# Optimization experiments

Hardware: AMD Instinct MI355X
Metric: run time of the kernel (lower is better)

## Reference

```python
import jax, jax.numpy as jnp
import numpy as np
from jax import lax

# Key identity used: modulating ALL weights of output channel o by s_o (with no bias
# inside the modulated conv, as in the source where F.conv2d(..., bias=None)) is
# mathematically identical to a plain conv followed by per-(batch, out_channel)
# scaling of the output. This collapses the per-sample Python loop into one conv.

def _upsample2x(x):
    # nearest-neighbor x2, matching F.interpolate(scale_factor=2) default mode
    return jnp.repeat(jnp.repeat(x, 2, axis=2), 2, axis=3)

def _conv(x, w):
    return lax.conv_general_dilated(
        x, w, window_strides=(1, 1), padding=[(1, 1), (1, 1)],
        dimension_numbers=("NCHW", "OIHW", "NCHW"))

def _modconv(x, style, w, fc_w, fc_b):
    # style_fc: [B, style_dim] -> [B, out_ch]
    s = style @ fc_w.T + fc_b          # [B, O]
    y = _conv(x, w)                    # [B, O, H, W]
    return y * s[:, :, None, None]


def setup_inputs() -> dict:
    key = jax.random.key(0)
    ks = jax.random.split(key, 16)
    B, SD = 8, 512
    chans = [(512, 256), (256, 128), (128, 64), (64, 64), (64, 64)]
    inp = {
        "x": jax.random.normal(ks[0], (B, 512, 8, 8), jnp.float32),
        "style": jax.random.normal(ks[1], (B, SD), jnp.float32),
    }
    for i, (ci, co) in enumerate(chans, start=1):
        inp[f"w{i}"] = jax.random.normal(ks[2 * i], (co, ci, 3, 3), jnp.float32) * (1.0 / np.sqrt(ci * 9))
        inp[f"fw{i}"] = jax.random.normal(ks[2 * i + 1], (co, SD), jnp.float32) * (1.0 / np.sqrt(SD))
        inp[f"fb{i}"] = jnp.ones((co,), jnp.float32)
    inp["wf"] = jax.random.normal(ks[12], (3, 64, 3, 3), jnp.float32) * (1.0 / np.sqrt(64 * 9))
    inp["bf"] = jnp.zeros((3,), jnp.float32)
    return inp


def reference(x, style, w1, fw1, fb1, w2, fw2, fb2, w3, fw3, fb3,
              w4, fw4, fb4, w5, fw5, fb5, wf, bf):
    x = _upsample2x(x)
    x = jax.nn.relu(_modconv(x, style, w1, fw1, fb1))
    x = _upsample2x(x)
    x = jax.nn.relu(_modconv(x, style, w2, fw2, fb2))
    x = _upsample2x(x)
    x = jax.nn.relu(_modconv(x, style, w3, fw3, fb3))
    x = _upsample2x(x)
    x = jax.nn.relu(_modconv(x, style, w4, fw4, fb4))
    x = _upsample2x(x)
    x = jax.nn.relu(_modconv(x, style, w5, fw5, fb5))
    x = _conv(x, wf) + bf[None, :, None, None]
    return x
```

## Files before the change

kernel.cpp:

```cpp
#include <hip/hip_runtime.h>
#include <hip/hip_bf16.h>
#include <cstddef>

typedef __bf16 bf16x8 __attribute__((ext_vector_type(8)));
typedef float f32x4 __attribute__((ext_vector_type(4)));

__global__ void prep_all_kernel(const float* __restrict__ x, __hip_bfloat16* __restrict__ act0,
                                const float* __restrict__ w1, __hip_bfloat16* __restrict__ o1,
                                const float* __restrict__ w2, __hip_bfloat16* __restrict__ o2,
                                const float* __restrict__ w3, __hip_bfloat16* __restrict__ o3,
                                const float* __restrict__ w4, __hip_bfloat16* __restrict__ o4,
                                const float* __restrict__ w5, __hip_bfloat16* __restrict__ o5,
                                const float* __restrict__ wf, __hip_bfloat16* __restrict__ of,
                                const float* __restrict__ style,
                                const float* __restrict__ fw1, const float* __restrict__ fb1,
                                const float* __restrict__ fw2, const float* __restrict__ fb2,
                                const float* __restrict__ fw3, const float* __restrict__ fb3,
                                const float* __restrict__ fw4, const float* __restrict__ fb4,
                                const float* __restrict__ fw5, const float* __restrict__ fb5,
                                float* __restrict__ S) {
    const int blk = blockIdx.x;
    if (blk < 1024) {
        int t = blk * 256 + threadIdx.x;
        int c = t & 511; int rest = t >> 9;
        int w = rest & 7; rest >>= 3; int h = rest & 7; int b = rest >> 3;
        act0[t] = __float2bfloat16(x[((b * 512 + c) * 8 + h) * 8 + w]);
    } else if (blk < 7620) {
        int t = (blk - 1024) * 256 + threadIdx.x;
        if (t >= 1688576) return;
        if (t < 1548288) {
            const float* w; __hip_bfloat16* o; int lgci, lgco;
            if      (t < 1179648) { w = w1; o = o1; lgci = 9; lgco = 8; }
            else if (t < 1474560) { t -= 1179648; w = w2; o = o2; lgci = 8; lgco = 7; }
            else                  { t -= 1474560; w = w3; o = o3; lgci = 7; lgco = 6; }
            int CI = 1 << lgci;
            int ci = t & (CI - 1);
            int co = (t >> lgci) & ((1 << lgco) - 1);
            int tap = t >> (lgci + lgco);
            o[t] = __float2bfloat16(w[((size_t)co * CI + ci) * 9 + tap]);
        } else if (t < 1679360) {
            int u = t - 1548288;
            const float* w; __hip_bfloat16* o;
            if (u < 65536) { w = w4; o = o4; }
            else           { u -= 65536; w = w5; o = o5; }
            int j   = u & 7;
            int ln  = (u >> 3) & 63;
            int ch  = (u >> 9) & 1;
            int nt  = (u >> 10) & 3;
            int tp  = (u >> 12) & 3;
            int cls = (u >> 14) & 3;
            int py = cls >> 1, px = cls & 1;
            int i = tp >> 1, jj = tp & 1;
            int co = nt * 16 + (ln & 15);
            int ci = ch * 32 + (ln >> 4) * 8 + j;
            int r0 = i * (1 + py), rc = py ? (2 - i) : (1 + i);
            int c0 = jj * (1 + px), cc = px ? (2 - jj) : (1 + jj);
            const float* wb = w + ((size_t)co * 64 + ci) * 9;
            float s = 0.f;
            for (int rr = 0; rr < rc; ++rr)
                for (int c2 = 0; c2 < cc; ++c2)
                    s += wb[(r0 + rr) * 3 + (c0 + c2)];
            o[u] = __float2bfloat16(s);
        } else {
            int u = t - 1679360;
            int j  = u & 7;
            int ln = (u >> 3) & 63;
            int ch = (u >> 9) & 1;
            int tap = u >> 10;
            int rr = ln & 15, qq = ln >> 4;
            int ci = ch * 32 + qq * 8 + j;
            float v = (rr < 3) ? wf[((size_t)rr * 64 + ci) * 9 + tap] : 0.f;
            of[u] = __float2bfloat16(v);
        }
    } else {
        int wvid = (blk - 7620) * 4 + (threadIdx.x >> 6);
        int lane = threadIdx.x & 63;
        const float* fw; const float* fb; int lg, sOff, local;
        if      (wvid < 2048) { fw = fw1; fb = fb1; lg = 8; sOff = 0;    local = wvid; }
        else if (wvid < 3072) { fw = fw2; fb = fb2; lg = 7; sOff = 2048; local = wvid - 2048; }
        else if (wvid < 3584) { fw = fw3; fb = fb3; lg = 6; sOff = 3072; local = wvid - 3072; }
        else if (wvid < 4096) { fw = fw4; fb = fb4; lg = 6; sOff = 3584; local = wvid - 3584; }
        else                  { fw = fw5; fb = fb5; lg = 6; sOff = 4096; local = wvid - 4096; }
        int b = local >> lg, o = local & ((1 << lg) - 1);
        const float* sb = style + b * 512;
        const float* fwo = fw + (size_t)o * 512;
        float p = 0.f;
        #pragma unroll
        for (int k = lane; k < 512; k += 64) p += sb[k] * fwo[k];
        #pragma unroll
        for (int off = 32; off > 0; off >>= 1) p += __shfl_down(p, off);
        if (lane == 0) S[sOff + local] = p + fb[o];
    }
}

template <int CI, int CO, int HS, int WS>
__launch_bounds__(512)
__global__ void conv_partial_kernel(const __hip_bfloat16* __restrict__ actIn,
                                    const __hip_bfloat16* __restrict__ wtr,
                                    float* __restrict__ Part) {
    constexpr int HO = HS * 2, WO = WS * 2;
    constexpr size_t sliceN = (size_t)8 * HO * WO * CO;
    const int tid = threadIdx.x;
    const int lane = tid & 63, wv = tid >> 6;
    const int r = lane & 15, q = lane >> 4;
    const int pw = WO / 16, ppb = (HO / 16) * pw;
    const int b = blockIdx.x / ppb;
    const int prest = blockIdx.x - b * ppb;
    const int ph = prest / pw, pwi = prest - ph * pw;
    const int oh0 = ph * 16, ow0 = pwi * 16;
    const int sh0 = oh0 >> 1, sw0 = ow0 >> 1;
    const int n0 = blockIdx.y * 64;
    const int ciOff = blockIdx.z * 64;

    __shared__ alignas(16) __hip_bfloat16 Tile[100 * 72];
    __shared__ alignas(16) __hip_bfloat16 Wlds[2][64 * 72];

    f32x4 acc[2][4];
    #pragma unroll
    for (int i = 0; i < 2; ++i)
        #pragma unroll
        for (int j = 0; j < 4; ++j) acc[i][j] = f32x4{0.f, 0.f, 0.f, 0.f};

    for (int i = tid; i < 800; i += 512) {
        int pix = i >> 3, koct = i & 7;
        int tr = pix / 10, tc2 = pix - tr * 10;
        int su = sh0 - 1 + tr, sv = sw0 - 1 + tc2;
        uint4 v = {0, 0, 0, 0};
        if (su >= 0 && su < HS && sv >= 0 && sv < WS)
            v = *(const uint4*)(actIn + ((size_t)((b * HS + su) * WS + sv) * CI + ciOff + koct * 8));
        *(uint4*)&Tile[pix * 72 + koct * 8] = v;
    }
    {
        int co = tid >> 3, koct = tid & 7;
        *(uint4*)&Wlds[0][co * 72 + koct * 8] =
            *(const uint4*)(wtr + ((size_t)(n0 + co)) * CI + ciOff + koct * 8);
    }
    __syncthreads();

    #pragma unroll 1
    for (int tap = 0; tap < 9; ++tap) {
        const bool pf = (tap < 8);
        uint4 wr0 = {0,0,0,0};
        if (pf) {
            int co0 = tid >> 3, k0 = tid & 7;
            wr0 = *(const uint4*)(wtr + ((size_t)(tap + 1) * CO + n0 + co0) * CI + ciOff + k0 * 8);
        }
        const int dyv = tap / 3;
        const int dxm1 = tap - dyv * 3 - 1;
        const int tc = ((r + dxm1) >> 1) + 1;
        int apix[2];
        #pragma unroll
        for (int mt = 0; mt < 2; ++mt)
            apix[mt] = ((((wv * 2 + mt) + dyv - 1) >> 1) + 1) * 10 + tc;

        const int buf = tap & 1;
        #pragma unroll
        for (int ch = 0; ch < 2; ++ch) {
            bf16x8 af[2], bfr[4];
            #pragma unroll
            for (int mt = 0; mt < 2; ++mt)
                af[mt] = *(const bf16x8*)&Tile[apix[mt] * 72 + ch * 32 + q * 8];
            #pragma unroll
            for (int nt = 0; nt < 4; ++nt)
                bfr[nt] = *(const bf16x8*)&Wlds[buf][(nt * 16 + r) * 72 + ch * 32 + q * 8];
            #pragma unroll
            for (int mt = 0; mt < 2; ++mt)
                #pragma unroll
                for (int nt = 0; nt < 4; ++nt)
                    acc[mt][nt] = __builtin_amdgcn_mfma_f32_16x16x32_bf16(
                        af[mt], bfr[nt], acc[mt][nt], 0, 0, 0);
        }
        if (pf) {
            int nb = buf ^ 1;
            int co0 = tid >> 3, k0 = tid & 7;
            *(uint4*)&Wlds[nb][co0 * 72 + k0 * 8] = wr0;
            __syncthreads();
        }
    }

    float* P = Part + (size_t)blockIdx.z * sliceN;
    #pragma unroll
    for (int mt = 0; mt < 2; ++mt) {
        const int prow = wv * 2 + mt;
        #pragma unroll
        for (int t2 = 0; t2 < 4; ++t2) {
            const int pcol = q * 4 + t2;
            const size_t obase = ((size_t)(b * HO + oh0 + prow) * WO + ow0 + pcol) * CO + n0;
            #pragma unroll
            for (int nt = 0; nt < 4; ++nt)
                P[obase + nt * 16 + r] = acc[mt][nt][t2];
        }
    }
}

template <int KS, int CO, int HW>
__launch_bounds__(256)
__global__ void reduce_kernel(const float* __restrict__ Part, const float* __restrict__ S,
                              __hip_bfloat16* __restrict__ actOut) {
    constexpr size_t sliceN = (size_t)8 * HW * CO;
    size_t e = ((size_t)blockIdx.x * 256 + threadIdx.x) * 4;
    if (e >= sliceN) return;
    f32x4 sum = {0.f, 0.f, 0.f, 0.f};
    #pragma unroll
    for (int k = 0; k < KS; ++k) sum += *(const f32x4*)(Part + (size_t)k * sliceN + e);
    const int co = (int)(e & (CO - 1));
    const int b = (int)(e / ((size_t)HW * CO));
    const float* Sb = S + b * CO + co;
    union { ushort4 u; __hip_bfloat16 h[4]; } pack;
    #pragma unroll
    for (int j = 0; j < 4; ++j)
        pack.h[j] = __float2bfloat16(fmaxf(sum[j] * Sb[j], 0.f));
    *(ushort4*)((unsigned short*)actOut + e) = pack.u;
}

template <int HS, int WS>
__launch_bounds__(256)
__global__ void conv_patch_kernel(const __hip_bfloat16* __restrict__ actIn,
                                  const __hip_bfloat16* __restrict__ wpk,
                                  const float* __restrict__ S,
                                  __hip_bfloat16* __restrict__ actOut) {
    constexpr int HO = HS * 2, WO = WS * 2;

    const int tid = threadIdx.x;
    const int lane = tid & 63, wv = tid >> 6;
    const int r = lane & 15, q = lane >> 4;
    const int rs = r >> 3, sc = r & 7;
    const int lane8 = lane * 8;
    const int py = wv >> 1, px = wv & 1;

    const int pw = WO / 16, ppb = (HO / 16) * pw;
    const int b = blockIdx.x / ppb;
    const int prest = blockIdx.x - b * ppb;
    const int ph = prest / pw, pwi = prest - ph * pw;
    const int oh0 = ph * 16, ow0 = pwi * 16;
    const int sh0 = oh0 >> 1, sw0 = ow0 >> 1;

    __shared__ alignas(16) __hip_bfloat16 Tile[100 * 72];

    f32x4 acc[4][4];
    #pragma unroll
    for (int i = 0; i < 4; ++i)
        #pragma unroll
        for (int j = 0; j < 4; ++j) acc[i][j] = f32x4{0.f, 0.f, 0.f, 0.f};

    for (int i = tid; i < 800; i += 256) {
        int pix = i >> 3, koct = i & 7;
        int tr = pix / 10, tc2 = pix - tr * 10;
        int su = sh0 - 1 + tr, sv = sw0 - 1 + tc2;
        uint4 v = {0, 0, 0, 0};
        if (su >= 0 && su < HS && sv >= 0 && sv < WS)
            v = *(const uint4*)(actIn + ((size_t)((b * HS + su) * WS + sv) * 64 + koct * 8));
        *(uint4*)&Tile[pix * 72 + koct * 8] = v;
    }
    __syncthreads();

    const __hip_bfloat16* wcls = wpk + ((size_t)wv << 14);

    bf16x8 bA[4][2], bB[4][2];

    auto loadB = [&](bf16x8 (&dst)[4][2], int tp) {
        #pragma unroll
        for (int nt = 0; nt < 4; ++nt)
            #pragma unroll
            for (int ch = 0; ch < 2; ++ch)
                dst[nt][ch] = *(const bf16x8*)(wcls + (tp << 12) + ((nt * 2 + ch) << 9) + lane8);
    };

    auto compute = [&](int tp, bf16x8 (&bfr)[4][2]) {
        const int i = tp >> 1, j = tp & 1;
        const int ro = i + py, co2 = j + px;
        int apix[4];
        #pragma unroll
        for (int mt = 0; mt < 4; ++mt)
            apix[mt] = (2 * mt + rs + ro) * 10 + (sc + co2);
        #pragma unroll
        for (int ch = 0; ch < 2; ++ch) {
            bf16x8 af[4];
            #pragma unroll
            for (int mt = 0; mt < 4; ++mt)
                af[mt] = *(const bf16x8*)&Tile[apix[mt] * 72 + ch * 32 + q * 8];
            #pragma unroll
            for (int mt = 0; mt < 4; ++mt)
                #pragma unroll
                for (int nt = 0; nt < 4; ++nt)
                    acc[mt][nt] = __builtin_amdgcn_mfma_f32_16x16x32_bf16(
                        af[mt], bfr[nt][ch], acc[mt][nt], 0, 0, 0);
        }
    };

    loadB(bA, 0);
    loadB(bB, 1);
    compute(0, bA);
    loadB(bA, 2);
    compute(1, bB);
    loadB(bB, 3);
    compute(2, bA);
    compute(3, bB);

    float sv_[4];
    #pragma unroll
    for (int nt = 0; nt < 4; ++nt) sv_[nt] = S[b * 64 + nt * 16 + r];
    #pragma unroll
    for (int mt = 0; mt < 4; ++mt) {
        #pragma unroll
        for (int t2 = 0; t2 < 4; ++t2) {
            const int m = q * 4 + t2;
            const int row = oh0 + 4 * mt + 2 * (m >> 3) + py;
            const int col = ow0 + 2 * (m & 7) + px;
            const size_t obase = ((size_t)(b * HO + row) * WO + col) * 64;
            #pragma unroll
            for (int nt = 0; nt < 4; ++nt)
                actOut[obase + nt * 16 + r] =
                    __float2bfloat16(fmaxf(acc[mt][nt][t2] * sv_[nt], 0.f));
        }
    }
}

__launch_bounds__(256)
__global__ void conv_final_kernel(const __hip_bfloat16* __restrict__ actIn,
                                  const __hip_bfloat16* __restrict__ wpkF,
                                  const float* __restrict__ bias,
                                  float* __restrict__ out) {
    constexpr int HO = 256, WO = 256;
    const int tid = threadIdx.x, lane = tid & 63, wv = tid >> 6;
    const int r = lane & 15, q = lane >> 4;
    const int lane8 = lane * 8;

    const int ppb = 32 * 16;
    const int b = blockIdx.x / ppb;
    const int prest = blockIdx.x - b * ppb;
    const int ph = prest >> 4, pwi = prest & 15;
    const int oh0 = ph * 8, ow0 = pwi * 16;

    __shared__ alignas(16) __hip_bfloat16 Tile[10 * 18 * 72];

    for (int i = tid; i < 1440; i += 256) {
        int pix = i >> 3, koct = i & 7;
        int tr = pix / 18, tc2 = pix - tr * 18;
        int u = oh0 - 1 + tr, v = ow0 - 1 + tc2;
        uint4 val = {0, 0, 0, 0};
        if (u >= 0 && u < HO && v >= 0 && v < WO)
            val = *(const uint4*)(actIn + ((size_t)((b * HO + u) * WO + v) * 64 + koct * 8));
        *(uint4*)&Tile[pix * 72 + koct * 8] = val;
    }
    __syncthreads();

    f32x4 acc[2];
    acc[0] = f32x4{0.f, 0.f, 0.f, 0.f};
    acc[1] = f32x4{0.f, 0.f, 0.f, 0.f};

    #pragma unroll 1
    for (int tap = 0; tap < 9; ++tap) {
        const int dyv = tap / 3;
        const int dxv = tap - dyv * 3;
        const int tc = r + dxv;
        int apix[2];
        #pragma unroll
        for (int mt = 0; mt < 2; ++mt)
            apix[mt] = (wv * 2 + mt + dyv) * 18 + tc;
        #pragma unroll
        for (int ch = 0; ch < 2; ++ch) {
            bf16x8 bfr = *(const bf16x8*)(wpkF + ((tap * 2 + ch) << 9) + lane8);
            #pragma unroll
            for (int mt = 0; mt < 2; ++mt) {
                bf16x8 af = *(const bf16x8*)&Tile[apix[mt] * 72 + ch * 32 + q * 8];
                acc[mt] = __builtin_amdgcn_mfma_f32_16x16x32_bf16(af, bfr, acc[mt], 0, 0, 0);
            }
        }
    }

    if (r < 3) {
        const float bs = bias[r];
        #pragma unroll
        for (int mt = 0; mt < 2; ++mt) {
            const int prow = wv * 2 + mt;
            #pragma unroll
            for (int t2 = 0; t2 < 4; ++t2) {
                const int pcol = q * 4 + t2;
                out[((size_t)(b * 3 + r) << 16) + (oh0 + prow) * 256 + ow0 + pcol] =
                    acc[mt][t2] + bs;
            }
        }
    }
}

extern "C" void kernel_launch(void* const* d_in, const int* in_sizes, int n_in,
                              void* d_out, int out_size, void* d_ws, size_t ws_size,
                              hipStream_t stream) {
    const float* x    = (const float*)d_in[0];
    const float* sty  = (const float*)d_in[1];
    const float* w1   = (const float*)d_in[2];
    const float* fw1  = (const float*)d_in[3];
    const float* fb1  = (const float*)d_in[4];
    const float* w2   = (const float*)d_in[5];
    const float* fw2  = (const float*)d_in[6];
    const float* fb2  = (const float*)d_in[7];
    const float* w3   = (const float*)d_in[8];
    const float* fw3  = (const float*)d_in[9];
    const float* fb3  = (const float*)d_in[10];
    const float* w4   = (const float*)d_in[11];
    const float* fw4  = (const float*)d_in[12];
    const float* fb4  = (const float*)d_in[13];
    const float* w5   = (const float*)d_in[14];
    const float* fw5  = (const float*)d_in[15];
    const float* fb5  = (const float*)d_in[16];
    const float* wf   = (const float*)d_in[17];
    const float* bf   = (const float*)d_in[18];
    float* out = (float*)d_out;

    char* ws = (char*)d_ws;
    size_t off = 0;
    auto alloc = [&](size_t bytes) {
        char* p = ws + off;
        off += (bytes + 255) & ~(size_t)255;
        return p;
    };
    float* S1 = (float*)alloc(8 * 256 * 4);
    float* S2 = (float*)alloc(8 * 128 * 4);
    float* S3 = (float*)alloc(8 * 64 * 4);
    float* S4 = (float*)alloc(8 * 64 * 4);
    float* S5 = (float*)alloc(8 * 64 * 4);
    __hip_bfloat16* act0 = (__hip_bfloat16*)alloc((size_t)262144 * 2);
    __hip_bfloat16* act1 = (__hip_bfloat16*)alloc((size_t)524288 * 2);
    __hip_bfloat16* act2 = (__hip_bfloat16*)alloc((size_t)1048576 * 2);
    __hip_bfloat16* act3 = (__hip_bfloat16*)alloc((size_t)2097152 * 2);
    __hip_bfloat16* act4 = (__hip_bfloat16*)alloc((size_t)8388608 * 2);
    __hip_bfloat16* act5 = (__hip_bfloat16*)alloc((size_t)33554432 * 2);
    __hip_bfloat16* wt1  = (__hip_bfloat16*)alloc((size_t)9 * 256 * 512 * 2);
    __hip_bfloat16* wt2  = (__hip_bfloat16*)alloc((size_t)9 * 128 * 256 * 2);
    __hip_bfloat16* wt3  = (__hip_bfloat16*)alloc((size_t)9 * 64 * 128 * 2);
    __hip_bfloat16* wt4  = (__hip_bfloat16*)alloc((size_t)65536 * 2);
    __hip_bfloat16* wt5  = (__hip_bfloat16*)alloc((size_t)65536 * 2);
    __hip_bfloat16* wtF  = (__hip_bfloat16*)alloc((size_t)9 * 16 * 64 * 2);
    if (off > ws_size) return;

    float* Part = (float*)act5;

    prep_all_kernel<<<8772, 256, 0, stream>>>(x, act0,
                                              w1, wt1, w2, wt2, w3, wt3,
                                              w4, wt4, w5, wt5, wf, wtF,
                                              sty, fw1, fb1, fw2, fb2, fw3, fb3,
                                              fw4, fb4, fw5, fb5, S1);

    conv_partial_kernel<512, 256, 8, 8><<<dim3(8, 4, 8), 512, 0, stream>>>(act0, wt1, Part);
    reduce_kernel<8, 256, 256><<<512, 256, 0, stream>>>(Part, S1, act1);
    conv_partial_kernel<256, 128, 16, 16><<<dim3(32, 2, 4), 512, 0, stream>>>(act1, wt2, Part);
    reduce_kernel<4, 128, 1024><<<1024, 256, 0, stream>>>(Part, S2, act2);
    conv_partial_kernel<128, 64, 32, 32><<<dim3(128, 1, 2), 512, 0, stream>>>(act2, wt3, Part);
    reduce_kernel<2, 64, 4096><<<2048, 256, 0, stream>>>(Part, S3, act3);

    conv_patch_kernel<64, 64><<<dim3(512), 256, 0, stream>>>(act3, wt4, S4, act4);
    conv_patch_kernel<128, 128><<<dim3(2048), 256, 0, stream>>>(act4, wt5, S5, act5);

    conv_final_kernel<<<4096, 256, 0, stream>>>(act5, wtF, bf, out);
}
```

Measured before the change: 213.8 us.

## Use subpixel-folded 2x2 weights for upsample convs in layers 1-3

Applies the nearest-upsample plus 3x3 conv folding (four parity classes, each a 2x2 conv with summed weights) to the first three conv_partial layers, as was already done for layers 4-5. This cuts MFMA work from 9 taps to 4 per output. Weights are now prepacked in MFMA fragment order and read straight from global into registers with double buffering, which removes the LDS weight staging and its barriers. The cost is a larger prep weight-packing phase and global B-fragment loads, which may be less coalesced or reused than the LDS path.

```diff
diff --git a/kernel.cpp b/kernel.cpp
--- a/kernel.cpp
+++ b/kernel.cpp
@@ -25,21 +25,34 @@
         int c = t & 511; int rest = t >> 9;
         int w = rest & 7; rest >>= 3; int h = rest & 7; int b = rest >> 3;
         act0[t] = __float2bfloat16(x[((b * 512 + c) * 8 + h) * 8 + w]);
-    } else if (blk < 7620) {
+    } else if (blk < 12324) {
         int t = (blk - 1024) * 256 + threadIdx.x;
-        if (t >= 1688576) return;
-        if (t < 1548288) {
-            const float* w; __hip_bfloat16* o; int lgci, lgco;
-            if      (t < 1179648) { w = w1; o = o1; lgci = 9; lgco = 8; }
-            else if (t < 1474560) { t -= 1179648; w = w2; o = o2; lgci = 8; lgco = 7; }
-            else                  { t -= 1474560; w = w3; o = o3; lgci = 7; lgco = 6; }
-            int CI = 1 << lgci;
-            int ci = t & (CI - 1);
-            int co = (t >> lgci) & ((1 << lgco) - 1);
-            int tap = t >> (lgci + lgco);
-            o[t] = __float2bfloat16(w[((size_t)co * CI + ci) * 9 + tap]);
-        } else if (t < 1679360) {
-            int u = t - 1548288;
+        if (t < 2752512) {
+            const float* w; __hip_bfloat16* o; int CI, lgCICH, lgCO16;
+            if      (t < 2097152) { w = w1; o = o1; CI = 512; lgCICH = 3; lgCO16 = 4; }
+            else if (t < 2621440) { t -= 2097152; w = w2; o = o2; CI = 256; lgCICH = 2; lgCO16 = 3; }
+            else                  { t -= 2621440; w = w3; o = o3; CI = 128; lgCICH = 1; lgCO16 = 2; }
+            int j    = t & 7;
+            int ln   = (t >> 3) & 63;
+            int ch   = (t >> 9) & 1;
+            int cich = (t >> 10) & ((1 << lgCICH) - 1);
+            int co16 = (t >> (10 + lgCICH)) & ((1 << lgCO16) - 1);
+            int tap  = (t >> (10 + lgCICH + lgCO16)) & 3;
+            int cls  = (t >> (12 + lgCICH + lgCO16)) & 3;
+            int co = co16 * 16 + (ln & 15);
+            int ci = cich * 64 + ch * 32 + (ln >> 4) * 8 + j;
+            int py = cls >> 1, px = cls & 1;
+            int i = tap >> 1, jj = tap & 1;
+            int r0 = i * (1 + py), rc = py ? (2 - i) : (1 + i);
+            int c0 = jj * (1 + px), cc = px ? (2 - jj) : (1 + jj);
+            const float* wb = w + ((size_t)co * CI + ci) * 9;
+            float s = 0.f;
+            for (int rr = 0; rr < rc; ++rr)
+                for (int c2 = 0; c2 < cc; ++c2)
+                    s += wb[(r0 + rr) * 3 + (c0 + c2)];
+            o[t] = __float2bfloat16(s);
+        } else if (t < 2883584) {
+            int u = t - 2752512;
             const float* w; __hip_bfloat16* o;
             if (u < 65536) { w = w4; o = o4; }
             else           { u -= 65536; w = w5; o = o5; }
@@ -61,8 +74,8 @@
                 for (int c2 = 0; c2 < cc; ++c2)
                     s += wb[(r0 + rr) * 3 + (c0 + c2)];
             o[u] = __float2bfloat16(s);
-        } else {
-            int u = t - 1679360;
+        } else if (t < 2892800) {
+            int u = t - 2883584;
             int j  = u & 7;
             int ln = (u >> 3) & 63;
             int ch = (u >> 9) & 1;
@@ -73,7 +86,7 @@
             of[u] = __float2bfloat16(v);
         }
     } else {
-        int wvid = (blk - 7620) * 4 + (threadIdx.x >> 6);
+        int wvid = (blk - 12324) * 4 + (threadIdx.x >> 6);
         int lane = threadIdx.x & 63;
         const float* fw; const float* fb; int lg, sOff, local;
         if      (wvid < 2048) { fw = fw1; fb = fb1; lg = 8; sOff = 0;    local = wvid; }
@@ -96,13 +109,20 @@
 template <int CI, int CO, int HS, int WS>
 __launch_bounds__(512)
 __global__ void conv_partial_kernel(const __hip_bfloat16* __restrict__ actIn,
-                                    const __hip_bfloat16* __restrict__ wtr,
+                                    const __hip_bfloat16* __restrict__ wpk,
                                     float* __restrict__ Part) {
     constexpr int HO = HS * 2, WO = WS * 2;
     constexpr size_t sliceN = (size_t)8 * HO * WO * CO;
+    constexpr int CICH = CI / 64, CO16 = CO / 16;
+
     const int tid = threadIdx.x;
     const int lane = tid & 63, wv = tid >> 6;
     const int r = lane & 15, q = lane >> 4;
+    const int rs = r >> 3, sc = r & 7;
+    const int lane8 = lane * 8;
+    const int cls = wv >> 1, half = wv & 1;
+    const int py = cls >> 1, px = cls & 1;
+
     const int pw = WO / 16, ppb = (HO / 16) * pw;
     const int b = blockIdx.x / ppb;
     const int prest = blockIdx.x - b * ppb;
@@ -110,10 +130,10 @@
     const int oh0 = ph * 16, ow0 = pwi * 16;
     const int sh0 = oh0 >> 1, sw0 = ow0 >> 1;
     const int n0 = blockIdx.y * 64;
-    const int ciOff = blockIdx.z * 64;
+    const int cich = blockIdx.z;
+    const int ciOff = cich * 64;
 
     __shared__ alignas(16) __hip_bfloat16 Tile[100 * 72];
-    __shared__ alignas(16) __hip_bfloat16 Wlds[2][64 * 72];
 
     f32x4 acc[2][4];
     #pragma unroll
@@ -130,62 +150,61 @@
             v = *(const uint4*)(actIn + ((size_t)((b * HS + su) * WS + sv) * CI + ciOff + koct * 8));
         *(uint4*)&Tile[pix * 72 + koct * 8] = v;
     }
-    {
-        int co = tid >> 3, koct = tid & 7;
-        *(uint4*)&Wlds[0][co * 72 + koct * 8] =
-            *(const uint4*)(wtr + ((size_t)(n0 + co)) * CI + ciOff + koct * 8);
-    }
     __syncthreads();
 
-    #pragma unroll 1
-    for (int tap = 0; tap < 9; ++tap) {
-        const bool pf = (tap < 8);
-        uint4 wr0 = {0,0,0,0};
-        if (pf) {
-            int co0 = tid >> 3, k0 = tid & 7;
-            wr0 = *(const uint4*)(wtr + ((size_t)(tap + 1) * CO + n0 + co0) * CI + ciOff + k0 * 8);
-        }
-        const int dyv = tap / 3;
-        const int dxm1 = tap - dyv * 3 - 1;
-        const int tc = ((r + dxm1) >> 1) + 1;
+    bf16x8 bA[4][2], bB[4][2];
+
+    auto loadB = [&](bf16x8 (&dst)[4][2], int tp) {
+        #pragma unroll
+        for (int nt = 0; nt < 4; ++nt) {
+            const int co16g = (n0 >> 4) + nt;
+            #pragma unroll
+            for (int ch = 0; ch < 2; ++ch)
+                dst[nt][ch] = *(const bf16x8*)(wpk +
+                    ((size_t)((((cls * 4 + tp) * CO16 + co16g) * CICH + cich) * 2 + ch) << 9) + lane8);
+        }
+    };
+
+    auto compute = [&](int tp, bf16x8 (&bfr)[4][2]) {
+        const int i = tp >> 1, j = tp & 1;
+        const int ro = i + py, co2 = j + px;
         int apix[2];
         #pragma unroll
         for (int mt = 0; mt < 2; ++mt)
-            apix[mt] = ((((wv * 2 + mt) + dyv - 1) >> 1) + 1) * 10 + tc;
-
-        const int buf = tap & 1;
+            apix[mt] = (2 * (half * 2 + mt) + rs + ro) * 10 + (sc + co2);
         #pragma unroll
         for (int ch = 0; ch < 2; ++ch) {
-            bf16x8 af[2], bfr[4];
+            bf16x8 af[2];
             #pragma unroll
             for (int mt = 0; mt < 2; ++mt)
                 af[mt] = *(const bf16x8*)&Tile[apix[mt] * 72 + ch * 32 + q * 8];
-            #pragma unroll
-            for (int nt = 0; nt < 4; ++nt)
-                bfr[nt] = *(const bf16x8*)&Wlds[buf][(nt * 16 + r) * 72 + ch * 32 + q * 8];
             #pragma unroll
             for (int mt = 0; mt < 2; ++mt)
                 #pragma unroll
                 for (int nt = 0; nt < 4; ++nt)
                     acc[mt][nt] = __builtin_amdgcn_mfma_f32_16x16x32_bf16(
-                        af[mt], bfr[nt], acc[mt][nt], 0, 0, 0);
-        }
-        if (pf) {
-            int nb = buf ^ 1;
-            int co0 = tid >> 3, k0 = tid & 7;
-            *(uint4*)&Wlds[nb][co0 * 72 + k0 * 8] = wr0;
-            __syncthreads();
-        }
-    }
+                        af[mt], bfr[nt][ch], acc[mt][nt], 0, 0, 0);
+        }
+    };
+
+    loadB(bA, 0);
+    loadB(bB, 1);
+    compute(0, bA);
+    loadB(bA, 2);
+    compute(1, bB);
+    loadB(bB, 3);
+    compute(2, bA);
+    compute(3, bB);
 
     float* P = Part + (size_t)blockIdx.z * sliceN;
     #pragma unroll
     for (int mt = 0; mt < 2; ++mt) {
-        const int prow = wv * 2 + mt;
         #pragma unroll
         for (int t2 = 0; t2 < 4; ++t2) {
-            const int pcol = q * 4 + t2;
-            const size_t obase = ((size_t)(b * HO + oh0 + prow) * WO + ow0 + pcol) * CO + n0;
+            const int m = q * 4 + t2;
+            const int row = oh0 + 2 * (2 * (half * 2 + mt) + (m >> 3)) + py;
+            const int col = ow0 + 2 * (m & 7) + px;
+            const size_t obase = ((size_t)(b * HO + row) * WO + col) * CO + n0;
             #pragma unroll
             for (int nt = 0; nt < 4; ++nt)
                 P[obase + nt * 16 + r] = acc[mt][nt][t2];
@@ -426,9 +445,9 @@
     __hip_bfloat16* act3 = (__hip_bfloat16*)alloc((size_t)2097152 * 2);
     __hip_bfloat16* act4 = (__hip_bfloat16*)alloc((size_t)8388608 * 2);
     __hip_bfloat16* act5 = (__hip_bfloat16*)alloc((size_t)33554432 * 2);
-    __hip_bfloat16* wt1  = (__hip_bfloat16*)alloc((size_t)9 * 256 * 512 * 2);
-    __hip_bfloat16* wt2  = (__hip_bfloat16*)alloc((size_t)9 * 128 * 256 * 2);
-    __hip_bfloat16* wt3  = (__hip_bfloat16*)alloc((size_t)9 * 64 * 128 * 2);
+    __hip_bfloat16* wt1  = (__hip_bfloat16*)alloc((size_t)2097152 * 2);
+    __hip_bfloat16* wt2  = (__hip_bfloat16*)alloc((size_t)524288 * 2);
+    __hip_bfloat16* wt3  = (__hip_bfloat16*)alloc((size_t)131072 * 2);
     __hip_bfloat16* wt4  = (__hip_bfloat16*)alloc((size_t)65536 * 2);
     __hip_bfloat16* wt5  = (__hip_bfloat16*)alloc((size_t)65536 * 2);
     __hip_bfloat16* wtF  = (__hip_bfloat16*)alloc((size_t)9 * 16 * 64 * 2);
@@ -436,11 +455,11 @@
 
     float* Part = (float*)act5;
 
-    prep_all_kernel<<<8772, 256, 0, stream>>>(x, act0,
-                                              w1, wt1, w2, wt2, w3, wt3,
-                                              w4, wt4, w5, wt5, wf, wtF,
-                                              sty, fw1, fb1, fw2, fb2, fw3, fb3,
-                                              fw4, fb4, fw5, fb5, S1);
+    prep_all_kernel<<<13476, 256, 0, stream>>>(x, act0,
+                                               w1, wt1, w2, wt2, w3, wt3,
+                                               w4, wt4, w5, wt5, wf, wtF,
+                                               sty, fw1, fb1, fw2, fb2, fw3, fb3,
+                                               fw4, fb4, fw5, fb5, S1);
 
     conv_partial_kernel<512, 256, 8, 8><<<dim3(8, 4, 8), 512, 0, stream>>>(act0, wt1, Part);
     reduce_kernel<8, 256, 256><<<512, 256, 0, stream>>>(Part, S1, act1);
```

Measured after the change: 212.3 us. Within noise of the previous version (-0.7%).
